# Kernel optimization log

Measured on AMD Instinct MI355X. Metric: run time of the kernel, lower is better.

## Reference

```python
import jax, jax.numpy as jnp
import numpy as np


def setup_inputs() -> dict:
    key = jax.random.key(0)
    k1, k2 = jax.random.split(key)
    B, S, D = 8, 4096, 1024
    E, P = 8, 4
    x = jax.random.normal(k1, (B, S, D), dtype=jnp.float32)
    phi_kernel = jax.random.normal(k2, (D, E * P), dtype=jnp.float32) * (1.0 / np.sqrt(D))
    phi_bias = jnp.zeros((E * P,), dtype=jnp.float32)
    return {"x": x, "phi_kernel": phi_kernel, "phi_bias": phi_bias,
            "num_experts": E, "num_slots": P}


def reference(x, phi_kernel, phi_bias, num_experts, num_slots):
    B, S, D = x.shape
    E, P = num_experts, num_slots
    # phi logits: [B,S,E,P]
    phi_logits = (jnp.einsum('bsd,dk->bsk', x, phi_kernel) + phi_bias).reshape(B, S, E, P)
    # softmax over the sequence axis (each slot is a convex combo of tokens)
    phi_weights = jax.nn.softmax(phi_logits, axis=1)
    # soft slots: weighted sum over tokens -> [B,E,P,D] (fused, no [B,S,E,P,D] blowup)
    soft_slots = jnp.einsum('bsd,bsep->bepd', x, phi_weights)
    expert_inputs = soft_slots.reshape(B, E, P * D)
    expert_weights = jnp.full((B, S, E), 1.0 / E, dtype=x.dtype)
    expert_indices = jnp.broadcast_to(jnp.arange(E, dtype=jnp.int32)[None, None, :], (B, S, E))
    return (expert_weights, expert_indices, phi_weights, soft_slots, expert_inputs)
```

## Files before the change

### kernel.cpp

```cpp
#include <hip/hip_runtime.h>
#include <hip/hip_bf16.h>

#define B 8
#define S 4096
#define DD 1024
#define KK 32

typedef __attribute__((ext_vector_type(8))) short bf16x8;
typedef __attribute__((ext_vector_type(16))) float f32x16;

static __device__ __forceinline__ unsigned short f2bf(float f) {
    unsigned int u = __builtin_bit_cast(unsigned int, f);
    u += 0x7FFFu + ((u >> 16) & 1u);
    return (unsigned short)(u >> 16);
}

static __device__ __forceinline__ unsigned int pack2bf(float lo, float hi) {
    return (unsigned int)f2bf(lo) | ((unsigned int)f2bf(hi) << 16);
}

static __device__ __forceinline__ void gload_lds16(const void* g, void* l) {
    __builtin_amdgcn_global_load_lds(
        (const __attribute__((address_space(1))) unsigned int*)g,
        (__attribute__((address_space(3))) unsigned int*)l, 16, 0, 0);
}

__global__ __launch_bounds__(256) void k0_phit(const float* __restrict__ phi,
                                               unsigned short* __restrict__ phiT) {
    __shared__ float lt[32][33];
    const int d0 = blockIdx.x * 32;
    const int tid = threadIdx.x;
#pragma unroll
    for (int i = 0; i < 4; ++i) {
        int slot = tid + i * 256;
        int d = slot >> 5, k = slot & 31;
        lt[d][k] = phi[(size_t)(d0 + d) * KK + k];
    }
    __syncthreads();
    const int k = tid >> 3, c = tid & 7, d = c * 4;
    short4 pk;
    pk.x = (short)f2bf(lt[d + 0][k]);
    pk.y = (short)f2bf(lt[d + 1][k]);
    pk.z = (short)f2bf(lt[d + 2][k]);
    pk.w = (short)f2bf(lt[d + 3][k]);
    *(short4*)(phiT + (size_t)k * DD + d0 + d) = pk;
}

__global__ __launch_bounds__(256) void k1_logits(const float* __restrict__ x,
                                                 const unsigned short* __restrict__ phiT,
                                                 const float* __restrict__ bias,
                                                 float* __restrict__ lp) {
    __shared__ __align__(16) char sm[32768];
    __shared__ float lt[32][129];

    const int bid = blockIdx.x;
    const int dq = bid & 1;
    const int st = (bid >> 1) & 31;
    const int b  = bid >> 6;
    const int tid = threadIdx.x;
    const int wv = __builtin_amdgcn_readfirstlane(tid >> 6);
    const int lane = tid & 63;
    const int l31 = lane & 31;
    const int half = lane >> 5;

    {
        const uint4* pg = (const uint4*)phiT;
#pragma unroll
        for (int i = 0; i < 8; ++i) {
            int slot = tid + i * 256;
            int k = slot >> 6, blk = slot & 63;
            uint4 v = pg[(size_t)k * 128 + dq * 64 + blk];
            *(uint4*)(sm + (size_t)k * 1024 + ((blk ^ (k & 7)) << 4)) = v;
        }
    }

    f32x16 acc;
    {
        float bv = (dq == 0) ? bias[l31] : 0.f;
#pragma unroll
        for (int r = 0; r < 16; ++r) acc[r] = bv;
    }
    __syncthreads();

    const float* xg = x + ((size_t)(b * S + st * 128 + wv * 32 + l31)) * DD
                        + dq * 512 + half * 8;
    const int kx = l31 & 7;
    const char* brow = sm + (size_t)l31 * 1024;

#pragma unroll 8
    for (int ch = 0; ch < 32; ++ch) {
        float4 a0 = *(const float4*)(xg + ch * 16);
        float4 a1 = *(const float4*)(xg + ch * 16 + 4);
        unsigned int p0 = pack2bf(a0.x, a0.y);
        unsigned int p1 = pack2bf(a0.z, a0.w);
        unsigned int p2 = pack2bf(a1.x, a1.y);
        unsigned int p3 = pack2bf(a1.z, a1.w);
        uint4 pv = make_uint4(p0, p1, p2, p3);
        bf16x8 af = __builtin_bit_cast(bf16x8, pv);
        bf16x8 bfv = *(const bf16x8*)(brow + (((ch * 2 + half) ^ kx) << 4));
        acc = __builtin_amdgcn_mfma_f32_32x32x16_bf16(af, bfv, acc, 0, 0, 0);
    }

#pragma unroll
    for (int r = 0; r < 16; ++r) {
        int row = (r & 3) + 8 * (r >> 2) + 4 * half;
        lt[l31][wv * 32 + row] = acc[r];
    }
    __syncthreads();
    float* o = lp + ((size_t)(dq * B + b) * KK) * S + st * 128;
#pragma unroll
    for (int i = 0; i < 4; ++i) {
        int slot = tid + i * 256;
        int k = slot >> 5, s4 = slot & 31;
        float4 v;
        v.x = lt[k][s4 * 4 + 0];
        v.y = lt[k][s4 * 4 + 1];
        v.z = lt[k][s4 * 4 + 2];
        v.w = lt[k][s4 * 4 + 3];
        *(float4*)(o + (size_t)k * S + s4 * 4) = v;
    }
}

__global__ __launch_bounds__(256) void k2a_partial(const float* __restrict__ lp,
                                                   float* __restrict__ pmax,
                                                   float* __restrict__ psum) {
    const int bid = blockIdx.x;
    const int c  = bid & 7;
    const int bk = bid >> 3;
    const int tid = threadIdx.x;
    const int wave = tid >> 6, lane = tid & 63;
    const size_t base = (size_t)bk * S + c * 512;

    float v0 = lp[base + tid]       + lp[1048576 + base + tid];
    float v1 = lp[base + tid + 256] + lp[1048576 + base + tid + 256];

    float m = fmaxf(v0, v1);
#pragma unroll
    for (int off = 32; off >= 1; off >>= 1) m = fmaxf(m, __shfl_xor(m, off, 64));
    __shared__ float sm_[4], sl[4];
    if (lane == 0) sm_[wave] = m;
    __syncthreads();
    const float M = fmaxf(fmaxf(sm_[0], sm_[1]), fmaxf(sm_[2], sm_[3]));

    float l = __expf(v0 - M) + __expf(v1 - M);
#pragma unroll
    for (int off = 32; off >= 1; off >>= 1) l += __shfl_xor(l, off, 64);
    if (lane == 0) sl[wave] = l;
    __syncthreads();
    if (tid == 0) {
        pmax[bid] = M;
        psum[bid] = sl[0] + sl[1] + sl[2] + sl[3];
    }
}

__global__ __launch_bounds__(256) void k2c_norm(const float* __restrict__ lp,
                                                const float* __restrict__ pmax,
                                                const float* __restrict__ psum,
                                                unsigned short* __restrict__ wbT,
                                                float* __restrict__ pw_out) {
    __shared__ float tile[128][33];
    __shared__ float sM[32], sLinv[32];
    const int b  = blockIdx.x >> 5;
    const int sc = blockIdx.x & 31;
    const int s0 = sc * 128;
    const int tid = threadIdx.x;

    if (tid < 32) {
        const int k = tid;
        float M = -1e30f, L = 0.f;
#pragma unroll
        for (int c = 0; c < 8; ++c) {
            float mc = pmax[(b * KK + k) * 8 + c];
            float lc = psum[(b * KK + k) * 8 + c];
            float nM = fmaxf(M, mc);
            L = L * __expf(M - nM) + lc * __expf(mc - nM);
            M = nM;
        }
        sM[k] = M;
        sLinv[k] = 1.0f / L;
    }
    __syncthreads();

    const int sL = tid & 127;
    const int kh = tid >> 7;
#pragma unroll
    for (int kk = 0; kk < 16; ++kk) {
        const int k = kk * 2 + kh;
        const size_t idx = ((size_t)b * KK + k) * S + s0 + sL;
        float v = lp[idx] + lp[1048576 + idx];
        float w = __expf(v - sM[k]) * sLinv[k];
        wbT[idx] = f2bf(w);
        tile[sL][k] = w;
    }
    __syncthreads();

    float* ob = pw_out + ((size_t)b * S + s0) * KK;
#pragma unroll
    for (int i = 0; i < 4; ++i) {
        const int idx4 = tid + i * 256;
        const int sl = idx4 >> 3, kq = idx4 & 7;
        float4 v4 = make_float4(tile[sl][kq * 4 + 0], tile[sl][kq * 4 + 1],
                                tile[sl][kq * 4 + 2], tile[sl][kq * 4 + 3]);
        ((float4*)ob)[idx4] = v4;
    }
}

__global__ __launch_bounds__(256) void k3_slots(const float* __restrict__ x,
                                                const unsigned short* __restrict__ wbT,
                                                float* __restrict__ part) {
    __shared__ __align__(16) char sm[2 * 32768 + 2 * 4096];

    const int bid = blockIdx.x;
    const int sc = bid & 7;
    const int dg = (bid >> 3) & 7;
    const int b  = bid >> 6;
    const int tid = threadIdx.x;
    const int wv = __builtin_amdgcn_readfirstlane(tid >> 6);
    const int lane = tid & 63;
    const int l31 = lane & 31;
    const int half = lane >> 5;

    const char* xsrc = (const char*)(x + ((size_t)(b * S + sc * 512 + wv * 16 + half)) * DD
                                       + dg * 128 + l31 * 4);
    const int wk = wv * 8 + (lane >> 3);
    const char* wsrc = (const char*)wbT + ((size_t)(b * KK + wk) * S + sc * 512) * 2
                                        + (((lane & 7) ^ (wk & 7)) << 4);

    char* const xb0 = sm;
    char* const wb0 = sm + 65536;

    auto stage = [&](int ch, int buf) {
        char* xb = xb0 + buf * 32768 + wv * (16 * 512);
        const char* xs = xsrc + (size_t)ch * (64 * DD * 4);
#pragma unroll
        for (int t = 0; t < 8; ++t)
            gload_lds16(xs + (size_t)t * (2 * DD * 4), xb + t * 1024);
        gload_lds16(wsrc + (size_t)ch * 128, wb0 + buf * 4096 + wv * 1024);
    };

    f32x16 acc;
#pragma unroll
    for (int r = 0; r < 16; ++r) acc[r] = 0.f;

    stage(0, 0);
    __syncthreads();

    const int col = wv * 32 + l31;
    const int kx = l31 & 7;

    for (int ch = 0; ch < 8; ++ch) {
        const int cur = ch & 1;
        if (ch < 7) stage(ch + 1, cur ^ 1);
        const float* xr = (const float*)(xb0 + cur * 32768);
        const char* wr = wb0 + cur * 4096 + (size_t)l31 * 128;
#pragma unroll
        for (int step = 0; step < 4; ++step) {
            bf16x8 af = *(const bf16x8*)(wr + (((step * 2 + half) ^ kx) << 4));
            const int sb = step * 16 + half * 8;
            unsigned int p0 = pack2bf(xr[(sb + 0) * 128 + col], xr[(sb + 1) * 128 + col]);
            unsigned int p1 = pack2bf(xr[(sb + 2) * 128 + col], xr[(sb + 3) * 128 + col]);
            unsigned int p2 = pack2bf(xr[(sb + 4) * 128 + col], xr[(sb + 5) * 128 + col]);
            unsigned int p3 = pack2bf(xr[(sb + 6) * 128 + col], xr[(sb + 7) * 128 + col]);
            uint4 pv = make_uint4(p0, p1, p2, p3);
            bf16x8 bfv = __builtin_bit_cast(bf16x8, pv);
            acc = __builtin_amdgcn_mfma_f32_32x32x16_bf16(af, bfv, acc, 0, 0, 0);
        }
        __syncthreads();
    }

    float* pp = part + (((size_t)sc * B + b) * KK) * DD + dg * 128 + col;
#pragma unroll
    for (int r = 0; r < 16; ++r) {
        int k = (r & 3) + 8 * (r >> 2) + 4 * half;
        pp[(size_t)k * DD] = acc[r];
    }
}

__global__ __launch_bounds__(256) void k4_finalize(const float* __restrict__ part,
                                                   float* __restrict__ out) {
    const int idx = blockIdx.x * 256 + threadIdx.x;
    const float4* p4 = (const float4*)part;

    float4 sv = p4[idx];
#pragma unroll
    for (int c = 1; c < 8; ++c) {
        float4 t = p4[(size_t)c * 65536 + idx];
        sv.x += t.x; sv.y += t.y; sv.z += t.z; sv.w += t.w;
    }

    ((float4*)(out + 1572864))[idx] = sv;
    ((float4*)(out + 1835008))[idx] = sv;
    ((float4*)out)[idx] = make_float4(0.125f, 0.125f, 0.125f, 0.125f);
    float base = (float)((idx * 4) & 7);
    ((float4*)(out + 262144))[idx] = make_float4(base, base + 1.f, base + 2.f, base + 3.f);
}

extern "C" void kernel_launch(void* const* d_in, const int* in_sizes, int n_in,
                              void* d_out, int out_size, void* d_ws, size_t ws_size,
                              hipStream_t stream) {
    const float* x    = (const float*)d_in[0];
    const float* phi  = (const float*)d_in[1];
    const float* bias = (const float*)d_in[2];
    float* out = (float*)d_out;

    float* ws = (float*)d_ws;
    float* lp   = ws;
    float* pmax = ws + 2097152;
    float* psum = ws + 2099200;
    unsigned short* wbT  = (unsigned short*)(ws + 2101248);
    unsigned short* phiT = (unsigned short*)(ws + 2625536);
    float* part = ws + 2641920;
    float* pw_out = out + 524288;

    k0_phit<<<dim3(32), dim3(256), 0, stream>>>(phi, phiT);
    k1_logits<<<dim3(512), dim3(256), 0, stream>>>(x, phiT, bias, lp);
    k2a_partial<<<dim3(2048), dim3(256), 0, stream>>>(lp, pmax, psum);
    k2c_norm<<<dim3(256), dim3(256), 0, stream>>>(lp, pmax, psum, wbT, pw_out);
    k3_slots<<<dim3(512), dim3(256), 0, stream>>>(x, wbT, part);
    k4_finalize<<<dim3(256), dim3(256), 0, stream>>>(part, out);
}
```

Baseline: 237.1 us.

## Drop D-split in logits kernel and fuse softmax partial stats into it

The logits kernel now has each block cover the full D=1024 reduction instead of splitting D across two blocks, so the two-way partial logits buffer and the extra adds downstream go away. Per-tile softmax max and sum-of-exp partials are computed from the LDS tile inside the logits kernel, which removes the separate partial-reduction kernel launch and its re-read of the logits. The trade-off is half as many blocks (256) with twice the LDS (64KB), which lowers parallelism and occupancy for the x-streaming GEMV. The normalization kernel now merges 32 partials per row instead of 8.

```diff
diff --git a/kernel.cpp b/kernel.cpp
--- a/kernel.cpp
+++ b/kernel.cpp
@@ -49,14 +49,14 @@
 __global__ __launch_bounds__(256) void k1_logits(const float* __restrict__ x,
                                                  const unsigned short* __restrict__ phiT,
                                                  const float* __restrict__ bias,
-                                                 float* __restrict__ lp) {
-    __shared__ __align__(16) char sm[32768];
-    __shared__ float lt[32][129];
+                                                 float* __restrict__ lp,
+                                                 float* __restrict__ pmax,
+                                                 float* __restrict__ psum) {
+    __shared__ __align__(16) char sm[65536];
 
     const int bid = blockIdx.x;
-    const int dq = bid & 1;
-    const int st = (bid >> 1) & 31;
-    const int b  = bid >> 6;
+    const int st = bid & 31;
+    const int b  = bid >> 5;
     const int tid = threadIdx.x;
     const int wv = __builtin_amdgcn_readfirstlane(tid >> 6);
     const int lane = tid & 63;
@@ -66,29 +66,28 @@
     {
         const uint4* pg = (const uint4*)phiT;
 #pragma unroll
-        for (int i = 0; i < 8; ++i) {
+        for (int i = 0; i < 16; ++i) {
             int slot = tid + i * 256;
-            int k = slot >> 6, blk = slot & 63;
-            uint4 v = pg[(size_t)k * 128 + dq * 64 + blk];
-            *(uint4*)(sm + (size_t)k * 1024 + ((blk ^ (k & 7)) << 4)) = v;
+            int k = slot >> 7, blk = slot & 127;
+            uint4 v = pg[(size_t)k * 128 + blk];
+            *(uint4*)(sm + (size_t)k * 2048 + ((blk ^ (k & 7)) << 4)) = v;
         }
     }
 
     f32x16 acc;
     {
-        float bv = (dq == 0) ? bias[l31] : 0.f;
+        float bv = bias[l31];
 #pragma unroll
         for (int r = 0; r < 16; ++r) acc[r] = bv;
     }
     __syncthreads();
 
-    const float* xg = x + ((size_t)(b * S + st * 128 + wv * 32 + l31)) * DD
-                        + dq * 512 + half * 8;
+    const float* xg = x + ((size_t)(b * S + st * 128 + wv * 32 + l31)) * DD + half * 8;
     const int kx = l31 & 7;
-    const char* brow = sm + (size_t)l31 * 1024;
+    const char* brow = sm + (size_t)l31 * 2048;
 
 #pragma unroll 8
-    for (int ch = 0; ch < 32; ++ch) {
+    for (int ch = 0; ch < 64; ++ch) {
         float4 a0 = *(const float4*)(xg + ch * 16);
         float4 a1 = *(const float4*)(xg + ch * 16 + 4);
         unsigned int p0 = pack2bf(a0.x, a0.y);
@@ -101,55 +100,43 @@
         acc = __builtin_amdgcn_mfma_f32_32x32x16_bf16(af, bfv, acc, 0, 0, 0);
     }
 
+    __syncthreads();
+    float* lt = (float*)sm;
 #pragma unroll
     for (int r = 0; r < 16; ++r) {
         int row = (r & 3) + 8 * (r >> 2) + 4 * half;
-        lt[l31][wv * 32 + row] = acc[r];
-    }
-    __syncthreads();
-    float* o = lp + ((size_t)(dq * B + b) * KK) * S + st * 128;
+        lt[(size_t)l31 * 129 + wv * 32 + row] = acc[r];
+    }
+    __syncthreads();
+
+    float* o = lp + ((size_t)b * KK) * S + st * 128;
 #pragma unroll
     for (int i = 0; i < 4; ++i) {
         int slot = tid + i * 256;
         int k = slot >> 5, s4 = slot & 31;
         float4 v;
-        v.x = lt[k][s4 * 4 + 0];
-        v.y = lt[k][s4 * 4 + 1];
-        v.z = lt[k][s4 * 4 + 2];
-        v.w = lt[k][s4 * 4 + 3];
+        v.x = lt[k * 129 + s4 * 4 + 0];
+        v.y = lt[k * 129 + s4 * 4 + 1];
+        v.z = lt[k * 129 + s4 * 4 + 2];
+        v.w = lt[k * 129 + s4 * 4 + 3];
         *(float4*)(o + (size_t)k * S + s4 * 4) = v;
     }
-}
-
-__global__ __launch_bounds__(256) void k2a_partial(const float* __restrict__ lp,
-                                                   float* __restrict__ pmax,
-                                                   float* __restrict__ psum) {
-    const int bid = blockIdx.x;
-    const int c  = bid & 7;
-    const int bk = bid >> 3;
-    const int tid = threadIdx.x;
-    const int wave = tid >> 6, lane = tid & 63;
-    const size_t base = (size_t)bk * S + c * 512;
-
-    float v0 = lp[base + tid]       + lp[1048576 + base + tid];
-    float v1 = lp[base + tid + 256] + lp[1048576 + base + tid + 256];
-
-    float m = fmaxf(v0, v1);
-#pragma unroll
-    for (int off = 32; off >= 1; off >>= 1) m = fmaxf(m, __shfl_xor(m, off, 64));
-    __shared__ float sm_[4], sl[4];
-    if (lane == 0) sm_[wave] = m;
-    __syncthreads();
-    const float M = fmaxf(fmaxf(sm_[0], sm_[1]), fmaxf(sm_[2], sm_[3]));
-
-    float l = __expf(v0 - M) + __expf(v1 - M);
-#pragma unroll
-    for (int off = 32; off >= 1; off >>= 1) l += __shfl_xor(l, off, 64);
-    if (lane == 0) sl[wave] = l;
-    __syncthreads();
-    if (tid == 0) {
-        pmax[bid] = M;
-        psum[bid] = sl[0] + sl[1] + sl[2] + sl[3];
+
+    const int pk = tid >> 3, pj = tid & 7;
+    const float* lr = lt + (size_t)pk * 129 + pj * 16;
+    float m = lr[0];
+#pragma unroll
+    for (int i = 1; i < 16; ++i) m = fmaxf(m, lr[i]);
+#pragma unroll
+    for (int off = 4; off >= 1; off >>= 1) m = fmaxf(m, __shfl_xor(m, off, 64));
+    float l = 0.f;
+#pragma unroll
+    for (int i = 0; i < 16; ++i) l += __expf(lr[i] - m);
+#pragma unroll
+    for (int off = 4; off >= 1; off >>= 1) l += __shfl_xor(l, off, 64);
+    if (pj == 0) {
+        pmax[((size_t)b * KK + pk) * 32 + st] = m;
+        psum[((size_t)b * KK + pk) * 32 + st] = l;
     }
 }
 
@@ -169,9 +156,9 @@
         const int k = tid;
         float M = -1e30f, L = 0.f;
 #pragma unroll
-        for (int c = 0; c < 8; ++c) {
-            float mc = pmax[(b * KK + k) * 8 + c];
-            float lc = psum[(b * KK + k) * 8 + c];
+        for (int c = 0; c < 32; ++c) {
+            float mc = pmax[((size_t)b * KK + k) * 32 + c];
+            float lc = psum[((size_t)b * KK + k) * 32 + c];
             float nM = fmaxf(M, mc);
             L = L * __expf(M - nM) + lc * __expf(mc - nM);
             M = nM;
@@ -187,7 +174,7 @@
     for (int kk = 0; kk < 16; ++kk) {
         const int k = kk * 2 + kh;
         const size_t idx = ((size_t)b * KK + k) * S + s0 + sL;
-        float v = lp[idx] + lp[1048576 + idx];
+        float v = lp[idx];
         float w = __expf(v - sM[k]) * sLinv[k];
         wbT[idx] = f2bf(w);
         tile[sL][k] = w;
@@ -305,16 +292,15 @@
 
     float* ws = (float*)d_ws;
     float* lp   = ws;
-    float* pmax = ws + 2097152;
-    float* psum = ws + 2099200;
-    unsigned short* wbT  = (unsigned short*)(ws + 2101248);
-    unsigned short* phiT = (unsigned short*)(ws + 2625536);
-    float* part = ws + 2641920;
+    float* pmax = ws + 1048576;
+    float* psum = ws + 1056768;
+    unsigned short* wbT  = (unsigned short*)(ws + 1064960);
+    unsigned short* phiT = (unsigned short*)(ws + 1589248);
+    float* part = ws + 1605632;
     float* pw_out = out + 524288;
 
     k0_phit<<<dim3(32), dim3(256), 0, stream>>>(phi, phiT);
-    k1_logits<<<dim3(512), dim3(256), 0, stream>>>(x, phiT, bias, lp);
-    k2a_partial<<<dim3(2048), dim3(256), 0, stream>>>(lp, pmax, psum);
+    k1_logits<<<dim3(256), dim3(256), 0, stream>>>(x, phiT, bias, lp, pmax, psum);
     k2c_norm<<<dim3(256), dim3(256), 0, stream>>>(lp, pmax, psum, wbT, pw_out);
     k3_slots<<<dim3(512), dim3(256), 0, stream>>>(x, wbT, part);
     k4_finalize<<<dim3(256), dim3(256), 0, stream>>>(part, out);
```

Measured after the change: 235.5 us. No clear change (-0.7%).
